# Optimization experiments

Hardware: AMD Instinct MI355X
Metric: run time of the kernel (lower is better)

Reference implementation:

```python
import jax, jax.numpy as jnp
import numpy as np

D_MODEL = 256
D_STATE = 32
D_CONV = 8
EXPAND = 4
D_INNER = EXPAND * D_MODEL  # 1024
DT_RANK = (D_MODEL + 15) // 16  # 16
EPS = 1e-5


def setup_inputs() -> dict:
    key = jax.random.key(0)
    ks = jax.random.split(key, 12)
    s = lambda *sh: 1.0 / np.sqrt(sh[-1])
    inp = {
        "x": jax.random.normal(ks[0], (8, 1024, D_MODEL), dtype=jnp.float32),
        "norm_w": jnp.ones((D_MODEL,), jnp.float32),
        "norm_b": jnp.zeros((D_MODEL,), jnp.float32),
        "in_proj_w": jax.random.normal(ks[1], (2 * D_INNER, D_MODEL), jnp.float32) * s(D_MODEL),
        "conv_w": jax.random.normal(ks[2], (D_INNER, 1, D_CONV), jnp.float32) * s(D_CONV),
        "conv_b": jax.random.normal(ks[3], (D_INNER,), jnp.float32) * 0.02,
        "x_proj_w": jax.random.normal(ks[4], (DT_RANK + 2 * D_STATE, D_INNER), jnp.float32) * s(D_INNER),
        "dt_proj_w": jax.random.normal(ks[5], (D_INNER, DT_RANK), jnp.float32) * s(DT_RANK),
        "dt_proj_b": jax.random.uniform(ks[6], (D_INNER,), jnp.float32, -4.0, -1.0),  # dt bias init
        "A_log": jnp.log(jnp.broadcast_to(jnp.arange(1, D_STATE + 1, dtype=jnp.float32), (D_INNER, D_STATE))),
        "D": jnp.ones((D_INNER,), jnp.float32),
        "out_proj_w": jax.random.normal(ks[7], (D_MODEL, D_INNER), jnp.float32) * s(D_INNER),
    }
    return inp


def _mamba_block(x, norm_w, norm_b, in_proj_w, conv_w, conv_b, x_proj_w,
                 dt_proj_w, dt_proj_b, A_log, D, out_proj_w):
    B_, L, _ = x.shape
    residual = x
    # LayerNorm
    mu = jnp.mean(x, -1, keepdims=True)
    var = jnp.mean(jnp.square(x - mu), -1, keepdims=True)
    xn = (x - mu) * jax.lax.rsqrt(var + EPS) * norm_w + norm_b
    # in_proj -> (u, z), each (B, L, D_INNER)
    xz = jnp.einsum("bld,ed->ble", xn, in_proj_w)
    u, z = jnp.split(xz, 2, axis=-1)
    # causal depthwise conv1d along L
    u_ncl = u.transpose(0, 2, 1)  # (B, D_INNER, L)
    u_conv = jax.lax.conv_general_dilated(
        u_ncl, conv_w, window_strides=(1,), padding=[(D_CONV - 1, 0)],
        feature_group_count=D_INNER, dimension_numbers=("NCH", "OIH", "NCH"))
    u_conv = u_conv + conv_b[None, :, None]
    u = jax.nn.silu(u_conv.transpose(0, 2, 1))  # (B, L, D_INNER)
    # x_proj -> dt, Bmat, Cmat
    x_dbl = jnp.einsum("bld,ed->ble", u, x_proj_w)
    dt, Bm, Cm = jnp.split(x_dbl, [DT_RANK, DT_RANK + D_STATE], axis=-1)
    delta = jax.nn.softplus(jnp.einsum("blr,dr->bld", dt, dt_proj_w) + dt_proj_b)
    A = -jnp.exp(A_log)  # (D_INNER, D_STATE)

    # selective scan over L; carry h: (B, D_INNER, D_STATE)
    def step(h, inp):
        d_t, B_t, C_t, u_t = inp  # (B,Di), (B,N), (B,N), (B,Di)
        dA = jnp.exp(d_t[..., None] * A)                       # (B,Di,N)
        dBu = d_t[..., None] * B_t[:, None, :] * u_t[..., None]
        h = dA * h + dBu
        y = jnp.einsum("bdn,bn->bd", h, C_t)
        return h, y

    xs = (delta.transpose(1, 0, 2), Bm.transpose(1, 0, 2),
          Cm.transpose(1, 0, 2), u.transpose(1, 0, 2))
    h0 = jnp.zeros((B_, D_INNER, D_STATE), delta.dtype)
    _, ys = jax.lax.scan(step, h0, xs)
    y = ys.transpose(1, 0, 2)  # (B, L, D_INNER)
    y = y + u * D
    y = y * jax.nn.silu(z)
    out = jnp.einsum("ble,de->bld", y, out_proj_w)
    # dropout is identity in eval mode
    return out + residual


def reference(x, norm_w, norm_b, in_proj_w, conv_w, conv_b, x_proj_w,
              dt_proj_w, dt_proj_b, A_log, D, out_proj_w):
    return _mamba_block(x, norm_w, norm_b, in_proj_w, conv_w, conv_b, x_proj_w,
                        dt_proj_w, dt_proj_b, A_log, D, out_proj_w)
```

## Files before the change

kernel.cpp:

```cpp
#include <hip/hip_runtime.h>
#include <hip/hip_bf16.h>
#include <math.h>


typedef float          f32x4 __attribute__((ext_vector_type(4)));
typedef short          s16x8 __attribute__((ext_vector_type(8)));
typedef unsigned short u16;
typedef u16            u16x4 __attribute__((ext_vector_type(4)));

#define DEV __device__ __forceinline__

DEV float bf2f(u16 u) { unsigned int i = ((unsigned int)u) << 16; return __builtin_bit_cast(float, i); }
DEV u16 f2bf(float f) {
  unsigned int x = __builtin_bit_cast(unsigned int, f);
  unsigned int r = (x + 0x7FFFu + ((x >> 16) & 1u)) >> 16;
  return (u16)r;
}
DEV float sigmoidf_(float x) { return 1.0f / (1.0f + __expf(-x)); }

__global__ void k_cast(const float* __restrict__ s, u16* __restrict__ d, int n) {
  int i = blockIdx.x * 256 + threadIdx.x;
  if (i < n) d[i] = f2bf(s[i]);
}
__global__ void k_pad_dtw(const float* __restrict__ s, u16* __restrict__ d) {
  int i = blockIdx.x * 256 + threadIdx.x;
  int row = i >> 5, k = i & 31;
  d[i] = (k < 16) ? f2bf(s[row * 16 + k]) : (u16)0;
}
__global__ void k_cast_dt(const float* __restrict__ xdbl, u16* __restrict__ d) {
  int i = blockIdx.x * 256 + threadIdx.x;
  int m = i >> 4, k = i & 15;
  d[i] = f2bf(xdbl[(size_t)m * 80 + k]);
}

__global__ __launch_bounds__(256) void k_ln(const float* __restrict__ x,
    const float* __restrict__ w, const float* __restrict__ b, u16* __restrict__ xn) {
  int row  = blockIdx.x * 4 + (threadIdx.x >> 6);
  int lane = threadIdx.x & 63;
  const float* xr = x + (size_t)row * 256 + lane * 4;
  f32x4 v = *(const f32x4*)xr;
  float s  = v[0] + v[1] + v[2] + v[3];
  float s2 = v[0]*v[0] + v[1]*v[1] + v[2]*v[2] + v[3]*v[3];
  for (int off = 32; off; off >>= 1) { s += __shfl_xor(s, off); s2 += __shfl_xor(s2, off); }
  float mu  = s * (1.0f / 256.0f);
  float inv = rsqrtf(s2 * (1.0f / 256.0f) - mu * mu + 1e-5f);
  int c = lane * 4;
  u16x4 o;
  #pragma unroll
  for (int t = 0; t < 4; ++t) o[t] = f2bf((v[t] - mu) * inv * w[c + t] + b[c + t]);
  *(u16x4*)(xn + (size_t)row * 256 + c) = o;
}

template<int WAVES_M, int WAVES_N, int WM, int WN, int EPI>
__global__ __launch_bounds__(WAVES_M * WAVES_N * 64)
void k_gemm(const u16* __restrict__ A, const u16* __restrict__ Bw,
            float* __restrict__ Cf, u16* __restrict__ Cb,
            const float* __restrict__ extra,
            int lda, int ldb, int ldc, int Ktiles, int Kact) {
  constexpr int BM = WAVES_M * WM * 16;
  constexpr int BN = WAVES_N * WN * 16;
  constexpr int BK = 32, LDP = BK + 8;
  constexpr int THREADS = WAVES_M * WAVES_N * 64;
  __shared__ u16 As[BM][LDP];
  __shared__ u16 Bs[BN][LDP];
  const int tid = threadIdx.x;
  const int m0 = blockIdx.x * BM, n0 = blockIdx.y * BN;
  const int w = tid >> 6, lane = tid & 63;
  const int wm = w / WAVES_N, wn = w % WAVES_N;
  const int r = lane & 15, kg = lane >> 4, ks = kg * 8;

  f32x4 acc[WM][WN] = {};

  for (int kt = 0; kt < Ktiles; ++kt) {
    const int k0 = kt * BK;
    for (int ci = tid; ci < BM * 4; ci += THREADS) {
      int row = ci >> 2, k8 = (ci & 3) * 8;
      s16x8 vv = {0, 0, 0, 0, 0, 0, 0, 0};
      if (k0 + k8 < Kact)
        vv = *(const s16x8*)(A + (size_t)(m0 + row) * lda + k0 + k8);
      *(s16x8*)(&As[row][k8]) = vv;
    }
    for (int ci = tid; ci < BN * 4; ci += THREADS) {
      int row = ci >> 2, k8 = (ci & 3) * 8;
      *(s16x8*)(&Bs[row][k8]) = *(const s16x8*)(Bw + (size_t)(n0 + row) * ldb + k0 + k8);
    }
    __syncthreads();
    s16x8 af[WM], bfr[WN];
    #pragma unroll
    for (int i = 0; i < WM; ++i) af[i]  = *(const s16x8*)(&As[wm * WM * 16 + i * 16 + r][ks]);
    #pragma unroll
    for (int j = 0; j < WN; ++j) bfr[j] = *(const s16x8*)(&Bs[wn * WN * 16 + j * 16 + r][ks]);
    #pragma unroll
    for (int i = 0; i < WM; ++i)
      #pragma unroll
      for (int j = 0; j < WN; ++j)
        acc[i][j] = __builtin_amdgcn_mfma_f32_16x16x32_bf16(af[i], bfr[j], acc[i][j], 0, 0, 0);
    __syncthreads();
  }

  #pragma unroll
  for (int i = 0; i < WM; ++i)
    #pragma unroll
    for (int j = 0; j < WN; ++j)
      #pragma unroll
      for (int q = 0; q < 4; ++q) {
        int gr = m0 + wm * WM * 16 + i * 16 + kg * 4 + q;
        int gc = n0 + wn * WN * 16 + j * 16 + r;
        float v = acc[i][j][q];
        size_t idx = (size_t)gr * ldc + gc;
        if constexpr (EPI == 0) Cf[idx] = v;
        else if constexpr (EPI == 1) Cb[idx] = f2bf(v);
        else if constexpr (EPI == 2) {
          v += extra[gc];
          v = (v > 20.0f) ? v : log1pf(expf(v));
          Cf[idx] = v;
        } else {
          Cf[idx] = v + extra[idx];
        }
      }
}

__global__ __launch_bounds__(256) void k_conv(const u16* __restrict__ xz,
    const float* __restrict__ cw, const float* __restrict__ cb, u16* __restrict__ u) {
  int d = (blockIdx.x & 3) * 256 + threadIdx.x;
  int m = blockIdx.x >> 2;
  int l = m & 1023;
  const f32x4* wv = (const f32x4*)(cw + (size_t)d * 8);
  f32x4 w0 = wv[0], w1 = wv[1];
  float acc = cb[d];
  #pragma unroll
  for (int j = 0; j < 8; ++j) {
    int li = l - 7 + j;
    float wj = (j < 4) ? w0[j] : w1[j - 4];
    if (li >= 0) acc = fmaf(bf2f(xz[(size_t)(m - 7 + j) * 2048 + d]), wj, acc);
  }
  u[(size_t)m * 1024 + d] = f2bf(acc * sigmoidf_(acc));
}

template<int C, int RM, bool BC>
DEV float dpp_add(float x) {
  int s = __builtin_amdgcn_update_dpp(0, __builtin_bit_cast(int, x), C, RM, 0xf, BC);
  return x + __builtin_bit_cast(float, s);
}

__global__ __launch_bounds__(256) void k_scan(const float* __restrict__ delta,
    const u16* __restrict__ u, const float* __restrict__ xdbl,
    const float* __restrict__ A_log, float* __restrict__ y) {
  constexpr int CH = 64, NC = 1024 / CH;
  __shared__ float sB[2][CH][32];
  __shared__ float sC[2][CH][32];
  __shared__ float sD[2][CH][8];
  __shared__ float sU[2][CH][8];
  const int b = blockIdx.x >> 7, dblk = blockIdx.x & 127;
  const int d0 = dblk * 8;
  const int t = threadIdx.x;
  const int n = t & 31, dloc = t >> 5;
  const int d = d0 + dloc;
  const float Adn = -__expf(A_log[d * 32 + n]) * 1.442695040888963f;
  const size_t mrow0 = (size_t)b * 1024;
  const int bcRow = t >> 5, bcCol = t & 31;
  const int dRow  = t >> 3, dCol  = t & 7;
  const int uRow  = t >> 2, uCol  = (t & 3) * 2;

  float rB[8], rC[8], rD[2], rU[2];

  auto load_chunk = [&](int c) {
    const int l0 = c * CH;
    #pragma unroll
    for (int i = 0; i < 8; ++i) {
      size_t m = mrow0 + l0 + bcRow + 8 * i;
      rB[i] = xdbl[m * 80 + 16 + bcCol];
      rC[i] = xdbl[m * 80 + 48 + bcCol];
    }
    #pragma unroll
    for (int i = 0; i < 2; ++i)
      rD[i] = delta[(mrow0 + l0 + dRow + 32 * i) * 1024 + d0 + dCol];
    const u16* up = u + (mrow0 + l0 + uRow) * 1024 + d0 + uCol;
    rU[0] = bf2f(up[0]); rU[1] = bf2f(up[1]);
  };
  auto write_chunk = [&](int buf) {
    #pragma unroll
    for (int i = 0; i < 8; ++i) {
      sB[buf][bcRow + 8 * i][bcCol] = rB[i];
      sC[buf][bcRow + 8 * i][bcCol] = rC[i];
    }
    #pragma unroll
    for (int i = 0; i < 2; ++i) sD[buf][dRow + 32 * i][dCol] = rD[i];
    sU[buf][uRow][uCol] = rU[0]; sU[buf][uRow][uCol + 1] = rU[1];
  };

  load_chunk(0);
  write_chunk(0);
  __syncthreads();

  float h = 0.0f;
  float* yp = y + mrow0 * 1024 + d;
  const bool writer = ((t & 31) == 31);
  for (int c = 0; c < NC; ++c) {
    const int cur = c & 1;
    if (c + 1 < NC) load_chunk(c + 1);
    const int l0 = c * CH;
    #pragma unroll 4
    for (int l = 0; l < CH; ++l) {
      float dv = sD[cur][l][dloc];
      float uv = sU[cur][l][dloc];
      float Bn = sB[cur][l][n];
      float Cn = sC[cur][l][n];
      float dA = exp2f(dv * Adn);
      h = fmaf(dA, h, dv * Bn * uv);
      float p = h * Cn;
      p = dpp_add<0x111, 0xf, true >(p);
      p = dpp_add<0x112, 0xf, true >(p);
      p = dpp_add<0x114, 0xf, true >(p);
      p = dpp_add<0x118, 0xf, true >(p);
      p = dpp_add<0x142, 0xa, false>(p);
      if (writer) yp[(size_t)(l0 + l) * 1024] = p;
    }
    if (c + 1 < NC) {
      write_chunk(cur ^ 1);
      __syncthreads();
    }
  }
}

__global__ __launch_bounds__(256) void k_yfinal(const float* __restrict__ y,
    const u16* __restrict__ u, const u16* __restrict__ xz,
    const float* __restrict__ Dv, u16* __restrict__ yb) {
  int i = blockIdx.x * 256 + threadIdx.x;
  int m = i >> 8, d = (i & 255) * 4;
  f32x4 yv = *(const f32x4*)(y + (size_t)m * 1024 + d);
  u16x4 uv = *(const u16x4*)(u + (size_t)m * 1024 + d);
  u16x4 zv = *(const u16x4*)(xz + (size_t)m * 2048 + 1024 + d);
  f32x4 Dw = *(const f32x4*)(Dv + d);
  u16x4 o;
  #pragma unroll
  for (int t = 0; t < 4; ++t) {
    float z = bf2f(zv[t]);
    float val = (yv[t] + bf2f(uv[t]) * Dw[t]) * (z * sigmoidf_(z));
    o[t] = f2bf(val);
  }
  *(u16x4*)(yb + (size_t)m * 1024 + d) = o;
}

extern "C" void kernel_launch(void* const* d_in, const int* in_sizes, int n_in,
                              void* d_out, int out_size, void* d_ws, size_t ws_size,
                              hipStream_t stream) {
  const float* x    = (const float*)d_in[0];
  const float* nw   = (const float*)d_in[1];
  const float* nb   = (const float*)d_in[2];
  const float* win  = (const float*)d_in[3];
  const float* cw   = (const float*)d_in[4];
  const float* cb   = (const float*)d_in[5];
  const float* wxp  = (const float*)d_in[6];
  const float* wdt  = (const float*)d_in[7];
  const float* dtb  = (const float*)d_in[8];
  const float* alog = (const float*)d_in[9];
  const float* Dv   = (const float*)d_in[10];
  const float* wout = (const float*)d_in[11];
  float* out = (float*)d_out;

  char* p = (char*)d_ws;
  auto alloc = [&](size_t bytes) { char* r = p; p += (bytes + 255) & ~(size_t)255; return r; };
  u16*   xn    = (u16*)  alloc((size_t)8192 * 256 * 2);
  u16*   winb  = (u16*)  alloc((size_t)2048 * 256 * 2);
  u16*   wxpb  = (u16*)  alloc((size_t)80 * 1024 * 2);
  u16*   wdtb  = (u16*)  alloc((size_t)1024 * 32 * 2);
  u16*   woutb = (u16*)  alloc((size_t)256 * 1024 * 2);
  u16*   xz    = (u16*)  alloc((size_t)8192 * 2048 * 2);
  u16*   ub    = (u16*)  alloc((size_t)8192 * 1024 * 2);
  float* xdbl  = (float*)alloc((size_t)8192 * 80 * 4);
  u16*   dtbf  = (u16*)  alloc((size_t)8192 * 16 * 2);
  float* delta = (float*)alloc((size_t)8192 * 1024 * 4);
  float* ysc   = (float*)alloc((size_t)8192 * 1024 * 4);
  u16*   ybf   = (u16*)  alloc((size_t)8192 * 1024 * 2);

  k_cast<<<2048, 256, 0, stream>>>(win, winb, 2048 * 256);
  k_cast<<<320, 256, 0, stream>>>(wxp, wxpb, 80 * 1024);
  k_pad_dtw<<<128, 256, 0, stream>>>(wdt, wdtb);
  k_cast<<<1024, 256, 0, stream>>>(wout, woutb, 256 * 1024);

  k_ln<<<2048, 256, 0, stream>>>(x, nw, nb, xn);
  k_gemm<2, 2, 4, 4, 1><<<dim3(64, 16), 256, 0, stream>>>(xn, winb, nullptr, xz, nullptr,
                                                          256, 256, 2048, 8, 256);
  k_conv<<<32768, 256, 0, stream>>>(xz, cw, cb, ub);
  k_gemm<2, 1, 1, 5, 0><<<dim3(256, 1), 128, 0, stream>>>(ub, wxpb, xdbl, nullptr, nullptr,
                                                          1024, 1024, 80, 32, 1024);
  k_cast_dt<<<512, 256, 0, stream>>>(xdbl, dtbf);
  k_gemm<2, 2, 4, 4, 2><<<dim3(64, 8), 256, 0, stream>>>(dtbf, wdtb, delta, nullptr, dtb,
                                                         16, 32, 1024, 1, 16);
  k_scan<<<1024, 256, 0, stream>>>(delta, ub, xdbl, alog, ysc);
  k_yfinal<<<8192, 256, 0, stream>>>(ysc, ub, xz, Dv, ybf);
  k_gemm<2, 2, 2, 2, 3><<<dim3(128, 4), 256, 0, stream>>>(ybf, woutb, out, nullptr, x,
                                                          1024, 1024, 256, 32, 1024);
}
```

Before: 439.8 us.

## Transpose delta and B/C for scan, precompute delta*u, fuse dt cast into x_proj epilogue

The x_proj GEMM epilogue now writes dt directly as bf16 and stores B and C transposed per batch as (state, L), which removes the separate cast kernel. The dt_proj epilogue writes delta transposed as (d, m) and also a precomputed delta*u buffer. This lets the scan read contiguous float4 runs along L per channel instead of staging delta and u through shared memory. The cost is scattered, uncoalesced transposed stores in the GEMM epilogues and an extra 32 MB buffer write.

```diff
diff --git a/kernel.cpp b/kernel.cpp
--- a/kernel.cpp
+++ b/kernel.cpp
@@ -26,11 +26,6 @@
   int i = blockIdx.x * 256 + threadIdx.x;
   int row = i >> 5, k = i & 31;
   d[i] = (k < 16) ? f2bf(s[row * 16 + k]) : (u16)0;
-}
-__global__ void k_cast_dt(const float* __restrict__ xdbl, u16* __restrict__ d) {
-  int i = blockIdx.x * 256 + threadIdx.x;
-  int m = i >> 4, k = i & 15;
-  d[i] = f2bf(xdbl[(size_t)m * 80 + k]);
 }
 
 __global__ __launch_bounds__(256) void k_ln(const float* __restrict__ x,
@@ -108,14 +103,19 @@
         int gc = n0 + wn * WN * 16 + j * 16 + r;
         float v = acc[i][j][q];
         size_t idx = (size_t)gr * ldc + gc;
-        if constexpr (EPI == 0) Cf[idx] = v;
-        else if constexpr (EPI == 1) Cb[idx] = f2bf(v);
-        else if constexpr (EPI == 2) {
+        if constexpr (EPI == 1) Cb[idx] = f2bf(v);
+        else if constexpr (EPI == 3) Cf[idx] = v + extra[idx];
+        else if constexpr (EPI == 4) {
+          int b_ = gr >> 10, l_ = gr & 1023;
+          if (gc < 16)      Cb[(size_t)gr * 16 + gc] = f2bf(v);
+          else if (gc < 48) Cf[(size_t)b_ * 32768 + (size_t)(gc - 16) * 1024 + l_] = v;
+          else              Cf[262144 + (size_t)b_ * 32768 + (size_t)(gc - 48) * 1024 + l_] = v;
+        } else if constexpr (EPI == 5) {
           v += extra[gc];
           v = (v > 20.0f) ? v : log1pf(expf(v));
-          Cf[idx] = v;
-        } else {
-          Cf[idx] = v + extra[idx];
+          size_t tidx = (size_t)gc * 8192 + gr;
+          Cf[tidx] = v;
+          Cf[8388608 + tidx] = v * bf2f(Cb[(size_t)gr * 1024 + gc]);
         }
       }
 }
@@ -143,78 +143,71 @@
   return x + __builtin_bit_cast(float, s);
 }
 
-__global__ __launch_bounds__(256) void k_scan(const float* __restrict__ delta,
-    const u16* __restrict__ u, const float* __restrict__ xdbl,
+__global__ __launch_bounds__(256) void k_scan(const float* __restrict__ deltaT,
+    const float* __restrict__ gT, const float* __restrict__ BC,
     const float* __restrict__ A_log, float* __restrict__ y) {
   constexpr int CH = 64, NC = 1024 / CH;
   __shared__ float sB[2][CH][32];
   __shared__ float sC[2][CH][32];
-  __shared__ float sD[2][CH][8];
-  __shared__ float sU[2][CH][8];
   const int b = blockIdx.x >> 7, dblk = blockIdx.x & 127;
   const int d0 = dblk * 8;
   const int t = threadIdx.x;
   const int n = t & 31, dloc = t >> 5;
   const int d = d0 + dloc;
   const float Adn = -__expf(A_log[d * 32 + n]) * 1.442695040888963f;
-  const size_t mrow0 = (size_t)b * 1024;
-  const int bcRow = t >> 5, bcCol = t & 31;
-  const int dRow  = t >> 3, dCol  = t & 7;
-  const int uRow  = t >> 2, uCol  = (t & 3) * 2;
-
-  float rB[8], rC[8], rD[2], rU[2];
-
+  const int stRow = t >> 3, stL = (t & 7) * 8;
+  const float* srcB = BC + (size_t)b * 32768;
+  const float* srcC = BC + 262144 + (size_t)b * 32768;
+
+  float rB[8], rC[8];
   auto load_chunk = [&](int c) {
     const int l0 = c * CH;
     #pragma unroll
     for (int i = 0; i < 8; ++i) {
-      size_t m = mrow0 + l0 + bcRow + 8 * i;
-      rB[i] = xdbl[m * 80 + 16 + bcCol];
-      rC[i] = xdbl[m * 80 + 48 + bcCol];
-    }
-    #pragma unroll
-    for (int i = 0; i < 2; ++i)
-      rD[i] = delta[(mrow0 + l0 + dRow + 32 * i) * 1024 + d0 + dCol];
-    const u16* up = u + (mrow0 + l0 + uRow) * 1024 + d0 + uCol;
-    rU[0] = bf2f(up[0]); rU[1] = bf2f(up[1]);
+      rB[i] = srcB[(size_t)stRow * 1024 + l0 + stL + i];
+      rC[i] = srcC[(size_t)stRow * 1024 + l0 + stL + i];
+    }
   };
   auto write_chunk = [&](int buf) {
     #pragma unroll
     for (int i = 0; i < 8; ++i) {
-      sB[buf][bcRow + 8 * i][bcCol] = rB[i];
-      sC[buf][bcRow + 8 * i][bcCol] = rC[i];
-    }
-    #pragma unroll
-    for (int i = 0; i < 2; ++i) sD[buf][dRow + 32 * i][dCol] = rD[i];
-    sU[buf][uRow][uCol] = rU[0]; sU[buf][uRow][uCol + 1] = rU[1];
+      sB[buf][stL + i][stRow] = rB[i];
+      sC[buf][stL + i][stRow] = rC[i];
+    }
   };
 
   load_chunk(0);
   write_chunk(0);
   __syncthreads();
 
+  const float* dTp = deltaT + (size_t)d * 8192 + (size_t)b * 1024;
+  const float* gTp = gT     + (size_t)d * 8192 + (size_t)b * 1024;
+  float* yp = y + ((size_t)b * 1024) * 1024 + d;
   float h = 0.0f;
-  float* yp = y + mrow0 * 1024 + d;
   const bool writer = ((t & 31) == 31);
   for (int c = 0; c < NC; ++c) {
     const int cur = c & 1;
     if (c + 1 < NC) load_chunk(c + 1);
-    const int l0 = c * CH;
-    #pragma unroll 4
-    for (int l = 0; l < CH; ++l) {
-      float dv = sD[cur][l][dloc];
-      float uv = sU[cur][l][dloc];
-      float Bn = sB[cur][l][n];
-      float Cn = sC[cur][l][n];
-      float dA = exp2f(dv * Adn);
-      h = fmaf(dA, h, dv * Bn * uv);
-      float p = h * Cn;
-      p = dpp_add<0x111, 0xf, true >(p);
-      p = dpp_add<0x112, 0xf, true >(p);
-      p = dpp_add<0x114, 0xf, true >(p);
-      p = dpp_add<0x118, 0xf, true >(p);
-      p = dpp_add<0x142, 0xa, false>(p);
-      if (writer) yp[(size_t)(l0 + l) * 1024] = p;
+    const int l0c = c * CH;
+    #pragma unroll 2
+    for (int l4 = 0; l4 < CH; l4 += 4) {
+      const int lg = l0c + l4;
+      f32x4 dv4 = *(const f32x4*)(dTp + lg);
+      f32x4 g4  = *(const f32x4*)(gTp + lg);
+      #pragma unroll
+      for (int j = 0; j < 4; ++j) {
+        float Bn = sB[cur][l4 + j][n];
+        float Cn = sC[cur][l4 + j][n];
+        float dA = exp2f(dv4[j] * Adn);
+        h = fmaf(dA, h, g4[j] * Bn);
+        float p = h * Cn;
+        p = dpp_add<0x111, 0xf, true >(p);
+        p = dpp_add<0x112, 0xf, true >(p);
+        p = dpp_add<0x114, 0xf, true >(p);
+        p = dpp_add<0x118, 0xf, true >(p);
+        p = dpp_add<0x142, 0xa, false>(p);
+        if (writer) yp[(size_t)(lg + j) * 1024] = p;
+      }
     }
     if (c + 1 < NC) {
       write_chunk(cur ^ 1);
@@ -268,9 +261,9 @@
   u16*   woutb = (u16*)  alloc((size_t)256 * 1024 * 2);
   u16*   xz    = (u16*)  alloc((size_t)8192 * 2048 * 2);
   u16*   ub    = (u16*)  alloc((size_t)8192 * 1024 * 2);
-  float* xdbl  = (float*)alloc((size_t)8192 * 80 * 4);
   u16*   dtbf  = (u16*)  alloc((size_t)8192 * 16 * 2);
-  float* delta = (float*)alloc((size_t)8192 * 1024 * 4);
+  float* bcbuf = (float*)alloc((size_t)2 * 8 * 32 * 1024 * 4);
+  float* dTgT  = (float*)alloc((size_t)2 * 8192 * 1024 * 4);
   float* ysc   = (float*)alloc((size_t)8192 * 1024 * 4);
   u16*   ybf   = (u16*)  alloc((size_t)8192 * 1024 * 2);
 
@@ -283,12 +276,11 @@
   k_gemm<2, 2, 4, 4, 1><<<dim3(64, 16), 256, 0, stream>>>(xn, winb, nullptr, xz, nullptr,
                                                           256, 256, 2048, 8, 256);
   k_conv<<<32768, 256, 0, stream>>>(xz, cw, cb, ub);
-  k_gemm<2, 1, 1, 5, 0><<<dim3(256, 1), 128, 0, stream>>>(ub, wxpb, xdbl, nullptr, nullptr,
+  k_gemm<2, 1, 1, 5, 4><<<dim3(256, 1), 128, 0, stream>>>(ub, wxpb, bcbuf, dtbf, nullptr,
                                                           1024, 1024, 80, 32, 1024);
-  k_cast_dt<<<512, 256, 0, stream>>>(xdbl, dtbf);
-  k_gemm<2, 2, 4, 4, 2><<<dim3(64, 8), 256, 0, stream>>>(dtbf, wdtb, delta, nullptr, dtb,
-                                                         16, 32, 1024, 1, 16);
-  k_scan<<<1024, 256, 0, stream>>>(delta, ub, xdbl, alog, ysc);
+  k_gemm<2, 2, 4, 4, 5><<<dim3(64, 8), 256, 0, stream>>>(dtbf, wdtb, dTgT, ub, dtb,
+                                                         16, 32, 8192, 1, 16);
+  k_scan<<<1024, 256, 0, stream>>>(dTgT, dTgT + 8388608, bcbuf, alog, ysc);
   k_yfinal<<<8192, 256, 0, stream>>>(ysc, ub, xz, Dv, ybf);
   k_gemm<2, 2, 2, 2, 3><<<dim3(128, 4), 256, 0, stream>>>(ybf, woutb, out, nullptr, x,
                                                           1024, 1024, 256, 32, 1024);
```

Measured after the change: 487.2 us. 1.11x slower.
